# Kernel optimization log

Hardware: AMD Instinct MI355X
Metric: run time of the kernel (lower is better)

## Reference

```python
import jax, jax.numpy as jnp
import numpy as np

N = 100000   # nodes
E = 800000   # edges
H = 128      # hidden_dim
HOP = 3
B = 64       # graphs


def setup_inputs() -> dict:
    key = jax.random.key(0)
    ks = jax.random.split(key, 24)
    s = 0.05
    x = jnp.round(jax.random.uniform(ks[0], (N, 1))).astype(jnp.float32)  # binary node indicator
    edge_index = jax.random.randint(ks[1], (2, E), 0, N)
    edge_attr = jax.random.normal(ks[2], (E, 1), dtype=jnp.float32)
    batch = jnp.sort(jax.random.randint(ks[3], (N,), 0, B))
    p = lambda k, sh: (s * jax.random.normal(k, sh)).astype(jnp.float32)
    return dict(
        x=x, edge_index=edge_index, edge_attr=edge_attr, batch=batch, num_graphs=B,
        l0_w=p(ks[4], (HOP, 1, H)), l0_b=p(ks[5], (HOP, H)),
        l1_w=p(ks[6], (HOP, H, H)), l1_b=p(ks[7], (HOP, H)),
        l2_w=p(ks[8], (HOP, 1, H)), l2_b=p(ks[9], (HOP, H)),
        l3_w=p(ks[10], (HOP, 1, 1)), l3_b=p(ks[11], (HOP, 1)),
        att_w=p(ks[12], (2 * H, H)), att_b=p(ks[13], (H,)),
        sp_w=p(ks[14], (H, H)), sp_b=p(ks[15], (H,)),
        ac_w=p(ks[16], (2 * H, H)), ac_b=p(ks[17], (H,)),
        last_w=p(ks[18], (2 * H, 1)), last_b=p(ks[19], (1,)),
    )


def _seg_mean(v, idx, m):
    # scatter-mean into m buckets; empty buckets -> 0 (matches PyG MeanAggregation)
    s = jax.ops.segment_sum(v, idx, num_segments=m)
    c = jax.ops.segment_sum(jnp.ones((v.shape[0], 1), v.dtype), idx, num_segments=m)
    return jnp.where(c > 0, s / jnp.maximum(c, 1.0), 0.0)


def reference(x, edge_index, edge_attr, batch, num_graphs,
              l0_w, l0_b, l1_w, l1_b, l2_w, l2_b, l3_w, l3_b,
              att_w, att_b, sp_w, sp_b, ac_w, ac_b, last_w, last_b):
    n = x.shape[0]
    row, col = edge_index[0], edge_index[1]
    hop, hid = l0_w.shape[0], l0_w.shape[2]
    u = jnp.zeros((n, hid), x.dtype)
    for i in range(hop):
        first = x @ l0_w[i] + l0_b[i]                      # [N,H]
        u_agg = _seg_mean(edge_attr * u[col], row, n)      # gather + scatter-mean
        second = u_agg @ l1_w[i] + l1_b[i]
        ee = jax.nn.relu(edge_attr @ l3_w[i] + l3_b[i])    # [E,1]
        third = _seg_mean(ee, row, n) @ l2_w[i] + l2_b[i]
        u = jax.nn.relu(first + second + third)
    # per-graph cluster embeddings (global_mean_pool ratios)
    h_c_0 = _seg_mean(u * (1 - x), batch, num_graphs) / _seg_mean(1 - x, batch, num_graphs)
    h_c_1 = _seg_mean(u * x, batch, num_graphs) / _seg_mean(x, batch, num_graphs)
    hc0, hc1 = h_c_0[batch], h_c_1[batch]                  # [N,H]
    tce = x * hc0 + (1 - x) * hc1
    h_a = jnp.concatenate([u, tce], axis=-1)               # [N,2H]
    att = h_a @ att_w + att_b
    w0 = jnp.sum(att * hc0, axis=1, keepdims=True)
    w1 = jnp.sum(att * hc1, axis=1, keepdims=True)
    w = jax.nn.softmax(jnp.concatenate([w0, w1], axis=-1), axis=-1)
    h_s = w[:, :1] * hc0 + w[:, 1:] * hc1
    q = jnp.concatenate([h_s @ sp_w + sp_b, h_a @ ac_w + ac_b], axis=-1) @ last_w + last_b
    return q
```

## Files before the change

kernel.cpp:

```cpp
#include <hip/hip_runtime.h>
#include <stdint.h>

typedef unsigned int  u32;
typedef unsigned short u16;
typedef unsigned char u8;

typedef short bf16x8 __attribute__((ext_vector_type(8)));
typedef float f32x4  __attribute__((ext_vector_type(4)));
typedef float f32x2  __attribute__((ext_vector_type(2)));

static __device__ __forceinline__ float b2f(u16 h){
    union { u32 u; float f; } v; v.u = ((u32)h) << 16; return v.f;
}
static __device__ __forceinline__ float b2f_hi(u32 w){
    union { u32 u; float f; } v; v.u = w & 0xFFFF0000u; return v.f;
}
static __device__ __forceinline__ float b2f_lo(u32 w){
    union { u32 u; float f; } v; v.u = w << 16; return v.f;
}
static __device__ __forceinline__ u16 f2b(float f){
    union { float f; u32 u; } v; v.f = f;
    u32 r = v.u + 0x7FFFu + ((v.u >> 16) & 1u);
    return (u16)(r >> 16);
}
static __device__ __forceinline__ u32 cvt_pk(float lo, float hi){
    u32 r; asm("v_cvt_pk_bf16_f32 %0, %1, %2" : "=v"(r) : "v"(lo), "v"(hi));
    return r;
}
static __device__ __forceinline__ u16 f2b1(float f){
    u32 r; asm("v_cvt_pk_bf16_f32 %0, %1, %2" : "=v"(r) : "v"(f), "v"(f));
    return (u16)r;
}

#define USCALE 64.0f
static __device__ __forceinline__ u32 pk8_lo(float a, float b, u32 old){
    return __builtin_amdgcn_cvt_pk_fp8_f32(a, b, old, false);
}
static __device__ __forceinline__ u32 pk8_hi(float a, float b, u32 old){
    return __builtin_amdgcn_cvt_pk_fp8_f32(a, b, old, true);
}
#define ACCF8(acc, g, v) { \
    f32x2 _a = __builtin_amdgcn_cvt_pk_f32_fp8((int)(v).x, false); \
    f32x2 _b = __builtin_amdgcn_cvt_pk_f32_fp8((int)(v).x, true);  \
    f32x2 _c = __builtin_amdgcn_cvt_pk_f32_fp8((int)(v).y, false); \
    f32x2 _d = __builtin_amdgcn_cvt_pk_f32_fp8((int)(v).y, true);  \
    acc[0] += g * _a[0]; acc[1] += g * _a[1]; \
    acc[2] += g * _b[0]; acc[3] += g * _b[1]; \
    acc[4] += g * _c[0]; acc[5] += g * _c[1]; \
    acc[6] += g * _d[0]; acc[7] += g * _d[1]; }

#define OL0W 0
#define OL0B 384
#define OL1W 768
#define OL1B 49920
#define OL2W 50304
#define OL2B 50688
#define OL3W 51072
#define OL3B 51075
#define OATTW 51078
#define OATTB 83846
#define OSPW 83974
#define OSPB 100358
#define OACW 100486
#define OACB 133254
#define OLASTW 133382
#define OLASTB 133638
#define WTOT 133639

#define PREPW_BLOCKS 192
#define ECAP 40

struct Ptrs16 { const void* p[16]; };

static __device__ __forceinline__ int detect_bf(const u32* __restrict__ xw){
    int lane = threadIdx.x & 63;
    int f = 0;
    #pragma unroll
    for (int i = 0; i < 8; ++i){
        u32 w = xw[lane * 8 + i];
        f |= ((w & 0xFFFFu) == 0x3F80u) ? 1 : 0;
    }
    return __ballot(f) != 0ull;
}

__global__ __launch_bounds__(256) void k_prep(Ptrs16 wp, const void* __restrict__ xin,
                                              float* __restrict__ wc, float* __restrict__ xc,
                                              u16* __restrict__ w1t, float* __restrict__ basev,
                                              int* __restrict__ flag,
                                              const int* __restrict__ row, const int* __restrict__ col,
                                              const void* __restrict__ ea,
                                              int* __restrict__ cnt, int2* __restrict__ ecs,
                                              int scatBase, int E, int N){
    int b = blockIdx.x, t = threadIdx.x;
    int bf = detect_bf((const u32*)xin);
    if (b >= scatBase){
        int e0 = ((b - scatBase) * 256 + t) * 4;
        if (e0 >= E) return;
        int rr[4], cc[4]; float av[4];
        if (e0 + 3 < E){
            int4 rv = *(const int4*)(row + e0);
            int4 cv = *(const int4*)(col + e0);
            rr[0]=rv.x; rr[1]=rv.y; rr[2]=rv.z; rr[3]=rv.w;
            cc[0]=cv.x; cc[1]=cv.y; cc[2]=cv.z; cc[3]=cv.w;
            if (bf){
                ushort4 ev = *(const ushort4*)((const u16*)ea + e0);
                av[0]=b2f(ev.x); av[1]=b2f(ev.y); av[2]=b2f(ev.z); av[3]=b2f(ev.w);
            } else {
                float4 ev = *(const float4*)((const float*)ea + e0);
                av[0]=ev.x; av[1]=ev.y; av[2]=ev.z; av[3]=ev.w;
            }
        } else {
            #pragma unroll
            for (int j = 0; j < 4; ++j){
                int e = e0 + j;
                rr[j] = (e < E) ? row[e] : 0;
                cc[j] = (e < E) ? col[e] : 0;
                av[j] = (e < E) ? (bf ? b2f(((const u16*)ea)[e]) : ((const float*)ea)[e]) : 0.f;
            }
        }
        int slot[4];
        #pragma unroll
        for (int j = 0; j < 4; ++j)
            slot[j] = (e0 + j < E) ? atomicAdd(&cnt[rr[j]], 1) : ECAP;
        #pragma unroll
        for (int j = 0; j < 4; ++j)
            if (e0 + j < E && slot[j] < ECAP)
                ecs[(size_t)rr[j] * ECAP + slot[j]] = make_int2(cc[j], __float_as_int(av[j]));
        return;
    }
    auto rd = [&](int seg, int off) -> float {
        return bf ? b2f(((const u16*)wp.p[seg])[off]) : ((const float*)wp.p[seg])[off];
    };
    if (b < PREPW_BLOCKS){
        int id = b * 256 + t;
        int i = id >> 14, rem = id & 16383;
        int n = rem >> 7, k = rem & 127;
        w1t[(i * 128 + n) * 128 + k] = f2b(rd(2, (i * 128 + k) * 128 + n));
        if (id < 384) basev[id] = rd(1, id) + rd(3, id) + rd(5, id);
        if (id == 0) *flag = bf;
    } else {
        int i = (b - PREPW_BLOCKS) * 256 + t;
        const int sz[16] = {384,384,49152,384,384,384,3,3,32768,128,16384,128,32768,128,256,1};
        if (i < WTOT){
            int seg = 0, off = i;
            while (off >= sz[seg]){ off -= sz[seg]; ++seg; }
            wc[i] = rd(seg, off);
        } else {
            int n = i - WTOT;
            if (n < N) xc[n] = bf ? b2f(((const u16*)xin)[n]) : ((const float*)xin)[n];
        }
    }
}

__global__ __launch_bounds__(256) void k_hop0(const int2* __restrict__ ecs, const int* __restrict__ cnt,
                                              const float* __restrict__ xc, const float* __restrict__ wc,
                                              float* __restrict__ t12, const float* __restrict__ basev,
                                              float* __restrict__ spf, float* __restrict__ acf,
                                              float* __restrict__ biasv,
                                              u8* __restrict__ uOut, int foldBlk, int N){
    if ((int)blockIdx.x == foldBlk){
        int t = threadIdx.x;
        const float* aw  = wc + OACW + t * 128;
        const float* lw2 = wc + OLASTW + 128;
        float s = 0.f;
        #pragma unroll 8
        for (int o = 0; o < 128; ++o) s += aw[o] * lw2[o];
        acf[t] = s;
        if (t < 128){
            const float* sw = wc + OSPW + t * 128;
            const float* lw = wc + OLASTW;
            float s2 = 0.f;
            #pragma unroll 8
            for (int o = 0; o < 128; ++o) s2 += sw[o] * lw[o];
            spf[t] = s2;
        }
        float pb = 0.f;
        if (t < 128) pb = wc[OSPB + t] * wc[OLASTW + t] + wc[OACB + t] * wc[OLASTW + 128 + t];
        __shared__ float red[4];
        #pragma unroll
        for (int m = 1; m < 64; m <<= 1) pb += __shfl_xor(pb, m);
        if ((t & 63) == 0) red[t >> 6] = pb;
        __syncthreads();
        if (t == 0) biasv[0] = red[0] + red[1] + red[2] + red[3] + wc[OLASTB];
        return;
    }
    int id = blockIdx.x * 256 + threadIdx.x;
    int n = id >> 4;
    if (n >= N) return;
    int sl = threadIdx.x & 15;
    float w30 = wc[OL3W + 0], w31 = wc[OL3W + 1], w32 = wc[OL3W + 2];
    float c30 = wc[OL3B + 0], c31 = wc[OL3B + 1], c32 = wc[OL3B + 2];
    int d = min(cnt[n], ECAP);
    size_t s = (size_t)n * ECAP;
    float s0 = 0.f, s1 = 0.f, s2 = 0.f;
    for (int e = sl; e < d; e += 16){
        float a = __int_as_float(ecs[s + e].y);
        s0 += fmaxf(a * w30 + c30, 0.f);
        s1 += fmaxf(a * w31 + c31, 0.f);
        s2 += fmaxf(a * w32 + c32, 0.f);
    }
    #pragma unroll
    for (int m = 1; m < 16; m <<= 1){
        s0 += __shfl_xor(s0, m);
        s1 += __shfl_xor(s1, m);
        s2 += __shfl_xor(s2, m);
    }
    float iv = d > 0 ? 1.0f / (float)d : 0.f;
    if (sl == 0){ t12[n] = s1 * iv; t12[N + n] = s2 * iv; }
    float t0 = s0 * iv;
    float xv = xc[n];
    int j = sl * 8;
    const float* l0wc = wc + OL0W;
    const float* l2wc = wc + OL2W;
    float vv[8];
    #pragma unroll
    for (int k = 0; k < 8; ++k)
        vv[k] = fmaxf(xv * l0wc[j + k] + t0 * l2wc[j + k] + basev[j + k], 0.f) * USCALE;
    u32 wlo = 0, whi = 0;
    wlo = pk8_lo(vv[0], vv[1], wlo); wlo = pk8_hi(vv[2], vv[3], wlo);
    whi = pk8_lo(vv[4], vv[5], whi); whi = pk8_hi(vv[6], vv[7], whi);
    *(uint2*)(uOut + (size_t)n * 128 + sl * 8) = make_uint2(wlo, whi);
}

template<int POOL, int OUTF8>
__global__ __launch_bounds__(256) void k_hop(const u8* __restrict__ uPrev, void* __restrict__ uNext,
    const int2* __restrict__ ecs, const int* __restrict__ cnt,
    const u16* __restrict__ w1t, const float* __restrict__ basev,
    const float* __restrict__ l0wc, const float* __restrict__ l2wc,
    const float* __restrict__ xc, const float* __restrict__ t_i,
    const int* __restrict__ batch, float* __restrict__ S0, float* __restrict__ S1,
    int* __restrict__ cnt1, int N)
{
    __shared__ __align__(16) u16 A[32][136];
    __shared__ __align__(8) int2 esh[32][17];
    __shared__ int dsh[32];
    int tid = threadIdx.x;
    int lane = tid & 63, wid = tid >> 6;
    int n0 = blockIdx.x * 32;
    int cid = lane & 15, grp = lane >> 4;

    {
        int sr = tid >> 3, sl = tid & 7;
        int sn = n0 + sr;
        if (sn < N){
            size_t sb = (size_t)sn * ECAP;
            esh[sr][sl]     = ecs[sb + sl];
            esh[sr][sl + 8] = ecs[sb + sl + 8];
            if (sl == 0) dsh[sr] = min(cnt[sn], ECAP);
        }
    }

    #pragma unroll
    for (int p = 0; p < 2; ++p){
        int r = wid * 8 + p * 4 + grp;
        int n = n0 + r;
        float acc[8];
        #pragma unroll
        for (int j = 0; j < 8; ++j) acc[j] = 0.f;
        if (n < N){
            int d = dsh[r];
            int m = min(d, 16);
            for (int e = 0; e < m; e += 4){
                int i1 = (e + 1 < m) ? e + 1 : 0;
                int i2 = (e + 2 < m) ? e + 2 : 0;
                int i3 = (e + 3 < m) ? e + 3 : 0;
                int2 m0 = esh[r][e], m1 = esh[r][i1], m2 = esh[r][i2], m3 = esh[r][i3];
                float g0 = __int_as_float(m0.y);
                float g1 = (e + 1 < m) ? __int_as_float(m1.y) : 0.f;
                float g2 = (e + 2 < m) ? __int_as_float(m2.y) : 0.f;
                float g3 = (e + 3 < m) ? __int_as_float(m3.y) : 0.f;
                uint2 p0 = *(const uint2*)(uPrev + (size_t)m0.x * 128 + cid * 8);
                uint2 p1 = *(const uint2*)(uPrev + (size_t)m1.x * 128 + cid * 8);
                uint2 p2 = *(const uint2*)(uPrev + (size_t)m2.x * 128 + cid * 8);
                uint2 p3 = *(const uint2*)(uPrev + (size_t)m3.x * 128 + cid * 8);
                ACCF8(acc, g0, p0); ACCF8(acc, g1, p1);
                ACCF8(acc, g2, p2); ACCF8(acc, g3, p3);
            }
            size_t s = (size_t)n * ECAP;
            for (int e = 16; e < d; ++e){
                int2 mm = ecs[s + e];
                float g = __int_as_float(mm.y);
                uint2 pp = *(const uint2*)(uPrev + (size_t)mm.x * 128 + cid * 8);
                ACCF8(acc, g, pp);
            }
            float sc = d > 0 ? 1.0f / (USCALE * (float)d) : 0.f;
            uint4 o;
            o.x = cvt_pk(acc[0] * sc, acc[1] * sc);
            o.y = cvt_pk(acc[2] * sc, acc[3] * sc);
            o.z = cvt_pk(acc[4] * sc, acc[5] * sc);
            o.w = cvt_pk(acc[6] * sc, acc[7] * sc);
            *(uint4*)&A[r][cid * 8] = o;
        } else {
            *(uint4*)&A[r][cid * 8] = make_uint4(0u, 0u, 0u, 0u);
        }
    }
    __syncthreads();

    bf16x8 bfr[4][2];
    #pragma unroll
    for (int kk = 0; kk < 4; ++kk)
        #pragma unroll
        for (int nt = 0; nt < 2; ++nt)
            bfr[kk][nt] = *(const bf16x8*)(w1t + (size_t)(wid * 32 + nt * 16 + cid) * 128 + kk * 32 + grp * 8);

    f32x4 acc4[2][2];
    #pragma unroll
    for (int mt = 0; mt < 2; ++mt)
        #pragma unroll
        for (int nt = 0; nt < 2; ++nt) acc4[mt][nt] = (f32x4){0.f, 0.f, 0.f, 0.f};
    #pragma unroll
    for (int kk = 0; kk < 4; ++kk){
        int kb = kk * 32 + grp * 8;
        bf16x8 af[2];
        #pragma unroll
        for (int mt = 0; mt < 2; ++mt) af[mt] = *(const bf16x8*)&A[mt * 16 + cid][kb];
        #pragma unroll
        for (int mt = 0; mt < 2; ++mt)
            #pragma unroll
            for (int nt = 0; nt < 2; ++nt)
                acc4[mt][nt] = __builtin_amdgcn_mfma_f32_16x16x32_bf16(af[mt], bfr[kk][nt], acc4[mt][nt], 0, 0, 0);
    }

    float w0c[2], w2c[2], bc[2]; int colv[2];
    #pragma unroll
    for (int nt = 0; nt < 2; ++nt){
        int col = wid * 32 + nt * 16 + cid;
        colv[nt] = col;
        w0c[nt] = l0wc[col]; w2c[nt] = l2wc[col]; bc[nt] = basev[col];
    }
    int gLo = 0, gHi = 0;
    float accP[8];
    if (POOL){
        gLo = batch[n0];
        gHi = batch[min(n0 + 31, N - 1)];
        #pragma unroll
        for (int j = 0; j < 8; ++j) accP[j] = 0.f;
    }
    #pragma unroll
    for (int mt = 0; mt < 2; ++mt){
        #pragma unroll
        for (int rg = 0; rg < 4; ++rg){
            int n = n0 + mt * 16 + grp * 4 + rg;
            if (n < N){
                float xv = xc[n];
                float tv = t_i[n];
                int sel = 0;
                if (POOL){
                    sel = ((batch[n] != gLo) ? 2 : 0) + ((xv > 0.5f) ? 1 : 0);
                }
                #pragma unroll
                for (int nt = 0; nt < 2; ++nt){
                    float v = fmaxf(acc4[mt][nt][rg] + xv * w0c[nt] + tv * w2c[nt] + bc[nt], 0.f);
                    if (OUTF8){
                        u32 pk = pk8_lo(v * USCALE, v * USCALE, 0u);
                        ((u8*)uNext)[(size_t)n * 128 + colv[nt]] = (u8)pk;
                    } else {
                        ((u16*)uNext)[(size_t)n * 128 + colv[nt]] = f2b1(v);
                    }
                    if (POOL) accP[nt * 4 + sel] += v;
                }
            }
        }
    }
    if (POOL){
        #pragma unroll
        for (int j = 0; j < 8; ++j){
            accP[j] += __shfl_xor(accP[j], 16);
            accP[j] += __shfl_xor(accP[j], 32);
        }
        if (grp == 0){
            #pragma unroll
            for (int nt = 0; nt < 2; ++nt){
                atomicAdd(&S0[gLo * 128 + colv[nt]], accP[nt * 4 + 0]);
                atomicAdd(&S1[gLo * 128 + colv[nt]], accP[nt * 4 + 1]);
                if (gHi != gLo){
                    atomicAdd(&S0[gHi * 128 + colv[nt]], accP[nt * 4 + 2]);
                    atomicAdd(&S1[gHi * 128 + colv[nt]], accP[nt * 4 + 3]);
                }
            }
        }
        if (wid == 0){
            int n = n0 + lane;
            int ok = (lane < 32 && n < N) ? 1 : 0;
            int is1 = ok && (xc[n] > 0.5f);
            int hi  = ok && (batch[n] != gLo);
            unsigned long long mLo = __ballot(is1 && !hi);
            unsigned long long mHi = __ballot(is1 && hi);
            if (lane == 0){
                int c = __popcll(mLo);
                if (c) atomicAdd(&cnt1[gLo], c);
                c = __popcll(mHi);
                if (c && gHi != gLo) atomicAdd(&cnt1[gHi], c);
            }
        }
    }
}


static __device__ __forceinline__ int lowbound(const int* b, int n, int g){
    int lo = 0, hi = n;
    while (lo < hi){ int m = (lo + hi) >> 1; if (b[m] < g) lo = m + 1; else hi = m; }
    return lo;
}

__global__ __launch_bounds__(256) void k_graph(const float* __restrict__ S0, const float* __restrict__ S1,
                                               const int* __restrict__ cnt1, const int* __restrict__ batch,
                                               const float* __restrict__ wc, const float* __restrict__ spf,
                                               const float* __restrict__ acf,
                                               float* __restrict__ v0, float* __restrict__ v1,
                                               float* __restrict__ gsc, int N){
    __shared__ float h0[128], h1[128], sv0[128], sv1[128];
    int g = blockIdx.x, t = threadIdx.x;
    int st = lowbound(batch, N, g), en = lowbound(batch, N, g + 1);
    int c1 = cnt1[g], c0 = (en - st) - c1;
    if (t < 128){
        h0[t] = c0 > 0 ? S0[g * 128 + t] / (float)c0 : 0.f;
        h1[t] = c1 > 0 ? S1[g * 128 + t] / (float)c1 : 0.f;
    }
    __syncthreads();
    float a0 = 0.f, a1 = 0.f;
    for (int o = 0; o < 128; ++o){
        float w = wc[OATTW + t * 128 + o];
        a0 += w * h0[o];
        a1 += w * h1[o];
    }
    v0[g * 256 + t] = a0; v1[g * 256 + t] = a1;
    if (t >= 128){ sv0[t - 128] = a0; sv1[t - 128] = a1; }
    __syncthreads();
    if (t < 64){
        int l = t;
        float p[10];
        #pragma unroll
        for (int k = 0; k < 10; ++k) p[k] = 0.f;
        #pragma unroll
        for (int rep = 0; rep < 2; ++rep){
            int o = l + rep * 64;
            float hh0 = h0[o], hh1 = h1[o];
            float q0 = sv0[o], q1 = sv1[o];
            float ab = wc[OATTB + o];
            float sf = spf[o], af = acf[128 + o];
            p[0] += q0 * hh0; p[1] += q0 * hh1;
            p[2] += q1 * hh0; p[3] += q1 * hh1;
            p[4] += ab * hh0; p[5] += ab * hh1;
            p[6] += sf * hh0; p[7] += sf * hh1;
            p[8] += af * hh0; p[9] += af * hh1;
        }
        #pragma unroll
        for (int m = 1; m < 64; m <<= 1){
            #pragma unroll
            for (int k = 0; k < 10; ++k) p[k] += __shfl_xor(p[k], m);
        }
        if (l == 0){
            #pragma unroll
            for (int k = 0; k < 10; ++k) gsc[g * 10 + k] = p[k];
        }
    }
}

__global__ __launch_bounds__(256) void k_final(const u16* __restrict__ u, const float* __restrict__ xc,
                                               const int* __restrict__ batch,
                                               const float* __restrict__ v0, const float* __restrict__ v1,
                                               const float* __restrict__ acf, const float* __restrict__ gsc,
                                               const float* __restrict__ biasv, const int* __restrict__ flag,
                                               void* __restrict__ out, int N){
    int bf = *flag;
    int lane = threadIdx.x & 63, wid = threadIdx.x >> 6;
    int sub = lane >> 4, cid = lane & 15;
    int n = blockIdx.x * 16 + wid * 4 + sub;
    if (n >= N) return;
    int g = batch[n];
    int ch = cid * 8;
    uint4 uv = *(const uint4*)(u + (size_t)n * 128 + ch);
    const float* pv0 = v0 + g * 256 + ch;
    const float* pv1 = v1 + g * 256 + ch;
    const float* pac = acf + ch;
    float uu[8] = {b2f_lo(uv.x), b2f_hi(uv.x), b2f_lo(uv.y), b2f_hi(uv.y),
                   b2f_lo(uv.z), b2f_hi(uv.z), b2f_lo(uv.w), b2f_hi(uv.w)};
    float r0 = 0.f, r1 = 0.f, rA = 0.f;
    #pragma unroll
    for (int j = 0; j < 8; ++j){ r0 += uu[j] * pv0[j]; r1 += uu[j] * pv1[j]; rA += uu[j] * pac[j]; }
    #pragma unroll
    for (int m = 1; m < 16; m <<= 1){
        r0 += __shfl_xor(r0, m);
        r1 += __shfl_xor(r1, m);
        rA += __shfl_xor(rA, m);
    }
    if (cid == 0){
        const float* G = gsc + g * 10;
        bool xv = xc[n] > 0.5f;
        float z0 = r0 + (xv ? G[0] : G[1]) + G[4];
        float z1 = r1 + (xv ? G[2] : G[3]) + G[5];
        float mz = fmaxf(z0, z1);
        float e0 = expf(z0 - mz), e1 = expf(z1 - mz);
        float inv = 1.f / (e0 + e1);
        float q = (e0 * G[6] + e1 * G[7]) * inv + rA + (xv ? G[8] : G[9]) + biasv[0];
        if (bf) ((u16*)out)[n] = f2b(q);
        else    ((float*)out)[n] = q;
    }
}


extern "C" void kernel_launch(void* const* d_in, const int* in_sizes, int n_in,
                              void* d_out, int out_size, void* d_ws, size_t ws_size,
                              hipStream_t stream)
{
    const void* x    = d_in[0];
    const int* ei    = (const int*)d_in[1];
    const void* ea   = d_in[2];
    const int* batch = (const int*)d_in[3];
    Ptrs16 wp;
    for (int i = 0; i < 16; ++i) wp.p[i] = d_in[5 + i];

    int N = in_sizes[0];
    int E = in_sizes[2];
    const int* rowI = ei;
    const int* colI = ei + E;

    char* w = (char*)d_ws;
    size_t o = 0;
    auto alloc = [&](size_t b) -> char* {
        char* p = w + o; o = (o + b + 255) & ~(size_t)255; return p;
    };
    int*   flag   = (int*)alloc(4);
    float* basev  = (float*)alloc(3 * 128 * 4);
    float* spf    = (float*)alloc(128 * 4);
    float* acf    = (float*)alloc(256 * 4);
    float* biasv  = (float*)alloc(4);
    float* gsc    = (float*)alloc(64 * 10 * 4);
    float* v0     = (float*)alloc(64 * 256 * 4);
    float* v1     = (float*)alloc(64 * 256 * 4);
    float* wc     = (float*)alloc((size_t)WTOT * 4);
    float* xc     = (float*)alloc((size_t)N * 4);
    float* t12    = (float*)alloc((size_t)2 * N * 4);
    u16*   w1t    = (u16*)alloc((size_t)3 * 128 * 128 * 2);
    u16*   uA     = (u16*)alloc((size_t)N * 128 * 2);
    u8*    uB     = (u8*)alloc((size_t)N * 128);
    int2*  ecs    = (int2*)alloc((size_t)N * ECAP * 8);
    int*   cnt    = (int*)alloc((size_t)N * 4);
    float* S0     = (float*)alloc(64 * 128 * 4);
    float* S1     = (float*)alloc(64 * 128 * 4);
    int*   cnt1   = (int*)alloc(64 * 4);
    (void)ws_size; (void)n_in; (void)out_size;

    hipMemsetAsync(cnt, 0, (size_t)((char*)cnt1 - (char*)cnt) + 64 * 4, stream);

    int gE4 = (E / 4 + 255) / 256 + 1;
    int canonB = (WTOT + N + 255) / 256;
    int scatBase = PREPW_BLOCKS + canonB;

    k_prep<<<scatBase + gE4, 256, 0, stream>>>(wp, x, wc, xc, w1t, basev, flag,
                                               rowI, colI, ea, cnt, ecs, scatBase, E, N);
    int gHop0 = (N * 16 + 255) / 256;
    k_hop0<<<gHop0 + 1, 256, 0, stream>>>(ecs, cnt, xc, wc, t12, basev, spf, acf, biasv,
                                          (u8*)uA, gHop0, N);

    int gHop = (N + 31) / 32;
    k_hop<0, 1><<<gHop, 256, 0, stream>>>((const u8*)uA, uB, ecs, cnt,
                                          w1t + 1 * 16384, basev + 128, wc + OL0W + 128, wc + OL2W + 128,
                                          xc, t12, batch, S0, S1, cnt1, N);
    k_hop<1, 0><<<gHop, 256, 0, stream>>>(uB, uA, ecs, cnt,
                                          w1t + 2 * 16384, basev + 256, wc + OL0W + 256, wc + OL2W + 256,
                                          xc, t12 + N, batch, S0, S1, cnt1, N);

    k_graph<<<64, 256, 0, stream>>>(S0, S1, cnt1, batch, wc, spf, acf, v0, v1, gsc, N);
    k_final<<<(N + 15) / 16, 256, 0, stream>>>(uA, xc, batch, v0, v1, acf, gsc, biasv, flag, d_out, N);
}
```

Baseline: 278.8 us.

## Recompute hop-0 features on the fly from packed scalars instead of materializing FP8 rows

Hop 0 no longer writes a 128-byte FP8 embedding per node. It stores one packed 32-bit value per node: the mean edge term with the binary x indicator in the sign bit. The first message-passing hop gathers that scalar per neighbor and rebuilds the 8 channels with relu(t*l2w + bias + x*l0w) in registers. This cuts the random-gather traffic from 8 bytes to 4 bytes per lane per edge and drops the hop-0 row writes, at the cost of extra ALU work per edge. It also stops quantizing the hop-0 features to FP8, which slightly changes numerics.

```diff
diff --git a/kernel.cpp b/kernel.cpp
--- a/kernel.cpp
+++ b/kernel.cpp
@@ -48,6 +48,15 @@
     acc[2] += g * _b[0]; acc[3] += g * _b[1]; \
     acc[4] += g * _c[0]; acc[5] += g * _c[1]; \
     acc[6] += g * _d[0]; acc[7] += g * _d[1]; }
+
+#define ACCP(acc, g, sv) { \
+    u32 _bb = __float_as_uint(sv); \
+    float _t = __uint_as_float(_bb & 0x7FFFFFFFu); \
+    bool _x = (_bb >> 31) != 0u; \
+    _Pragma("unroll") \
+    for (int _k = 0; _k < 8; ++_k){ \
+        float _v = fmaxf(fmaf(_t, cl2[_k], _x ? cb1[_k] : cb0[_k]), 0.f); \
+        acc[_k] = fmaf(g, _v, acc[_k]); } }
 
 #define OL0W 0
 #define OL0B 384
@@ -154,10 +163,9 @@
 
 __global__ __launch_bounds__(256) void k_hop0(const int2* __restrict__ ecs, const int* __restrict__ cnt,
                                               const float* __restrict__ xc, const float* __restrict__ wc,
-                                              float* __restrict__ t12, const float* __restrict__ basev,
-                                              float* __restrict__ spf, float* __restrict__ acf,
-                                              float* __restrict__ biasv,
-                                              u8* __restrict__ uOut, int foldBlk, int N){
+                                              float* __restrict__ t12, float* __restrict__ spf,
+                                              float* __restrict__ acf, float* __restrict__ biasv,
+                                              float* __restrict__ xt0, int foldBlk, int N){
     if ((int)blockIdx.x == foldBlk){
         int t = threadIdx.x;
         const float* aw  = wc + OACW + t * 128;
@@ -206,27 +214,19 @@
         s2 += __shfl_xor(s2, m);
     }
     float iv = d > 0 ? 1.0f / (float)d : 0.f;
-    if (sl == 0){ t12[n] = s1 * iv; t12[N + n] = s2 * iv; }
-    float t0 = s0 * iv;
-    float xv = xc[n];
-    int j = sl * 8;
-    const float* l0wc = wc + OL0W;
-    const float* l2wc = wc + OL2W;
-    float vv[8];
-    #pragma unroll
-    for (int k = 0; k < 8; ++k)
-        vv[k] = fmaxf(xv * l0wc[j + k] + t0 * l2wc[j + k] + basev[j + k], 0.f) * USCALE;
-    u32 wlo = 0, whi = 0;
-    wlo = pk8_lo(vv[0], vv[1], wlo); wlo = pk8_hi(vv[2], vv[3], wlo);
-    whi = pk8_lo(vv[4], vv[5], whi); whi = pk8_hi(vv[6], vv[7], whi);
-    *(uint2*)(uOut + (size_t)n * 128 + sl * 8) = make_uint2(wlo, whi);
-}
-
-template<int POOL, int OUTF8>
-__global__ __launch_bounds__(256) void k_hop(const u8* __restrict__ uPrev, void* __restrict__ uNext,
+    if (sl == 0){
+        t12[n] = s1 * iv; t12[N + n] = s2 * iv;
+        u32 tb = __float_as_uint(s0 * iv) | (xc[n] > 0.5f ? 0x80000000u : 0u);
+        ((u32*)xt0)[n] = tb;
+    }
+}
+
+template<int POOL, int OUTF8, int INPARAM>
+__global__ __launch_bounds__(256) void k_hop(const void* __restrict__ uPrevV, void* __restrict__ uNext,
     const int2* __restrict__ ecs, const int* __restrict__ cnt,
     const u16* __restrict__ w1t, const float* __restrict__ basev,
     const float* __restrict__ l0wc, const float* __restrict__ l2wc,
+    const float* __restrict__ p0c, const float* __restrict__ p2c, const float* __restrict__ pbc,
     const float* __restrict__ xc, const float* __restrict__ t_i,
     const int* __restrict__ batch, float* __restrict__ S0, float* __restrict__ S1,
     int* __restrict__ cnt1, int N)
@@ -238,6 +238,19 @@
     int lane = tid & 63, wid = tid >> 6;
     int n0 = blockIdx.x * 32;
     int cid = lane & 15, grp = lane >> 4;
+    const u8* uPrev = (const u8*)uPrevV;
+    const float* xt0 = (const float*)uPrevV;
+
+    float cl2[8], cb0[8], cb1[8];
+    if (INPARAM){
+        #pragma unroll
+        for (int k = 0; k < 8; ++k){
+            int ch = cid * 8 + k;
+            cl2[k] = p2c[ch];
+            float b = pbc[ch];
+            cb0[k] = b; cb1[k] = b + p0c[ch];
+        }
+    }
 
     {
         int sr = tid >> 3, sl = tid & 7;
@@ -260,30 +273,53 @@
         if (n < N){
             int d = dsh[r];
             int m = min(d, 16);
-            for (int e = 0; e < m; e += 4){
-                int i1 = (e + 1 < m) ? e + 1 : 0;
-                int i2 = (e + 2 < m) ? e + 2 : 0;
-                int i3 = (e + 3 < m) ? e + 3 : 0;
-                int2 m0 = esh[r][e], m1 = esh[r][i1], m2 = esh[r][i2], m3 = esh[r][i3];
-                float g0 = __int_as_float(m0.y);
-                float g1 = (e + 1 < m) ? __int_as_float(m1.y) : 0.f;
-                float g2 = (e + 2 < m) ? __int_as_float(m2.y) : 0.f;
-                float g3 = (e + 3 < m) ? __int_as_float(m3.y) : 0.f;
-                uint2 p0 = *(const uint2*)(uPrev + (size_t)m0.x * 128 + cid * 8);
-                uint2 p1 = *(const uint2*)(uPrev + (size_t)m1.x * 128 + cid * 8);
-                uint2 p2 = *(const uint2*)(uPrev + (size_t)m2.x * 128 + cid * 8);
-                uint2 p3 = *(const uint2*)(uPrev + (size_t)m3.x * 128 + cid * 8);
-                ACCF8(acc, g0, p0); ACCF8(acc, g1, p1);
-                ACCF8(acc, g2, p2); ACCF8(acc, g3, p3);
+            if (INPARAM){
+                for (int e = 0; e < m; e += 4){
+                    int i1 = (e + 1 < m) ? e + 1 : 0;
+                    int i2 = (e + 2 < m) ? e + 2 : 0;
+                    int i3 = (e + 3 < m) ? e + 3 : 0;
+                    int2 m0 = esh[r][e], m1 = esh[r][i1], m2 = esh[r][i2], m3 = esh[r][i3];
+                    float g0 = __int_as_float(m0.y);
+                    float g1 = (e + 1 < m) ? __int_as_float(m1.y) : 0.f;
+                    float g2 = (e + 2 < m) ? __int_as_float(m2.y) : 0.f;
+                    float g3 = (e + 3 < m) ? __int_as_float(m3.y) : 0.f;
+                    float q0 = xt0[m0.x], q1 = xt0[m1.x], q2 = xt0[m2.x], q3 = xt0[m3.x];
+                    ACCP(acc, g0, q0); ACCP(acc, g1, q1);
+                    ACCP(acc, g2, q2); ACCP(acc, g3, q3);
+                }
+                size_t s = (size_t)n * ECAP;
+                for (int e = 16; e < d; ++e){
+                    int2 mm = ecs[s + e];
+                    float g = __int_as_float(mm.y);
+                    float q = xt0[mm.x];
+                    ACCP(acc, g, q);
+                }
+            } else {
+                for (int e = 0; e < m; e += 4){
+                    int i1 = (e + 1 < m) ? e + 1 : 0;
+                    int i2 = (e + 2 < m) ? e + 2 : 0;
+                    int i3 = (e + 3 < m) ? e + 3 : 0;
+                    int2 m0 = esh[r][e], m1 = esh[r][i1], m2 = esh[r][i2], m3 = esh[r][i3];
+                    float g0 = __int_as_float(m0.y);
+                    float g1 = (e + 1 < m) ? __int_as_float(m1.y) : 0.f;
+                    float g2 = (e + 2 < m) ? __int_as_float(m2.y) : 0.f;
+                    float g3 = (e + 3 < m) ? __int_as_float(m3.y) : 0.f;
+                    uint2 p0 = *(const uint2*)(uPrev + (size_t)m0.x * 128 + cid * 8);
+                    uint2 p1 = *(const uint2*)(uPrev + (size_t)m1.x * 128 + cid * 8);
+                    uint2 p2 = *(const uint2*)(uPrev + (size_t)m2.x * 128 + cid * 8);
+                    uint2 p3 = *(const uint2*)(uPrev + (size_t)m3.x * 128 + cid * 8);
+                    ACCF8(acc, g0, p0); ACCF8(acc, g1, p1);
+                    ACCF8(acc, g2, p2); ACCF8(acc, g3, p3);
+                }
+                size_t s = (size_t)n * ECAP;
+                for (int e = 16; e < d; ++e){
+                    int2 mm = ecs[s + e];
+                    float g = __int_as_float(mm.y);
+                    uint2 pp = *(const uint2*)(uPrev + (size_t)mm.x * 128 + cid * 8);
+                    ACCF8(acc, g, pp);
+                }
             }
-            size_t s = (size_t)n * ECAP;
-            for (int e = 16; e < d; ++e){
-                int2 mm = ecs[s + e];
-                float g = __int_as_float(mm.y);
-                uint2 pp = *(const uint2*)(uPrev + (size_t)mm.x * 128 + cid * 8);
-                ACCF8(acc, g, pp);
-            }
-            float sc = d > 0 ? 1.0f / (USCALE * (float)d) : 0.f;
+            float sc = d > 0 ? (INPARAM ? 1.0f / (float)d : 1.0f / (USCALE * (float)d)) : 0.f;
             uint4 o;
             o.x = cvt_pk(acc[0] * sc, acc[1] * sc);
             o.y = cvt_pk(acc[2] * sc, acc[3] * sc);
@@ -532,6 +568,7 @@
     float* wc     = (float*)alloc((size_t)WTOT * 4);
     float* xc     = (float*)alloc((size_t)N * 4);
     float* t12    = (float*)alloc((size_t)2 * N * 4);
+    float* xt0    = (float*)alloc((size_t)N * 4);
     u16*   w1t    = (u16*)alloc((size_t)3 * 128 * 128 * 2);
     u16*   uA     = (u16*)alloc((size_t)N * 128 * 2);
     u8*    uB     = (u8*)alloc((size_t)N * 128);
@@ -551,16 +588,18 @@
     k_prep<<<scatBase + gE4, 256, 0, stream>>>(wp, x, wc, xc, w1t, basev, flag,
                                                rowI, colI, ea, cnt, ecs, scatBase, E, N);
     int gHop0 = (N * 16 + 255) / 256;
-    k_hop0<<<gHop0 + 1, 256, 0, stream>>>(ecs, cnt, xc, wc, t12, basev, spf, acf, biasv,
-                                          (u8*)uA, gHop0, N);
+    k_hop0<<<gHop0 + 1, 256, 0, stream>>>(ecs, cnt, xc, wc, t12, spf, acf, biasv,
+                                          xt0, gHop0, N);
 
     int gHop = (N + 31) / 32;
-    k_hop<0, 1><<<gHop, 256, 0, stream>>>((const u8*)uA, uB, ecs, cnt,
-                                          w1t + 1 * 16384, basev + 128, wc + OL0W + 128, wc + OL2W + 128,
-                                          xc, t12, batch, S0, S1, cnt1, N);
-    k_hop<1, 0><<<gHop, 256, 0, stream>>>(uB, uA, ecs, cnt,
-                                          w1t + 2 * 16384, basev + 256, wc + OL0W + 256, wc + OL2W + 256,
-                                          xc, t12 + N, batch, S0, S1, cnt1, N);
+    k_hop<0, 1, 1><<<gHop, 256, 0, stream>>>(xt0, uB, ecs, cnt,
+                                             w1t + 1 * 16384, basev + 128, wc + OL0W + 128, wc + OL2W + 128,
+                                             wc + OL0W, wc + OL2W, basev,
+                                             xc, t12, batch, S0, S1, cnt1, N);
+    k_hop<1, 0, 0><<<gHop, 256, 0, stream>>>(uB, uA, ecs, cnt,
+                                             w1t + 2 * 16384, basev + 256, wc + OL0W + 256, wc + OL2W + 256,
+                                             wc + OL0W, wc + OL2W, basev,
+                                             xc, t12 + N, batch, S0, S1, cnt1, N);
 
     k_graph<<<64, 256, 0, stream>>>(S0, S1, cnt1, batch, wc, spf, acf, v0, v1, gsc, N);
     k_final<<<(N + 15) / 16, 256, 0, stream>>>(uA, xc, batch, v0, v1, acf, gsc, biasv, flag, d_out, N);
```

Result: no change. 277.2 us (-0.6%).
